# Performance work log

Measured on AMD Instinct MI355X. Metric: run time of the kernel, lower is better.

## Reference

```python
import jax, jax.numpy as jnp
import numpy as np

N_NODES = 50000
N_EDGES = 200000
NODE_DIM = 32   # in_channels (== hidden_dim, required by NNConv nn output size)
EDGE_DIM = 16
HIDDEN = 32
OUT_DIM = 32
EPS = 1e-5
SLOPE = 0.01  # LeakyReLU default negative_slope


def setup_inputs() -> dict:
    key = jax.random.key(0)
    ks = jax.random.split(key, 16)
    inp = {
        "x": jax.random.normal(ks[0], (N_NODES, NODE_DIM), dtype=jnp.float32),
        "edge_index": jax.random.randint(ks[1], (2, N_EDGES), 0, N_NODES, dtype=jnp.int64),
        "edge_attr": jax.random.normal(ks[2], (N_EDGES, EDGE_DIM), dtype=jnp.float32),
        "batch": jnp.zeros((N_NODES,), dtype=jnp.int64),
        # edge MLP params
        "W1": jax.random.normal(ks[3], (EDGE_DIM, HIDDEN), dtype=jnp.float32) / np.sqrt(EDGE_DIM),
        "b1": jnp.zeros((HIDDEN,), dtype=jnp.float32),
        "bn1_gamma": jnp.ones((HIDDEN,), dtype=jnp.float32),
        "bn1_beta": jnp.zeros((HIDDEN,), dtype=jnp.float32),
        "bn1_mean": jax.random.normal(ks[4], (HIDDEN,), dtype=jnp.float32) * 0.1,
        "bn1_var": jax.random.uniform(ks[5], (HIDDEN,), dtype=jnp.float32, minval=0.5, maxval=1.5),
        "W2": jax.random.normal(ks[6], (HIDDEN, HIDDEN * OUT_DIM), dtype=jnp.float32) / np.sqrt(HIDDEN),
        "b2": jnp.zeros((HIDDEN * OUT_DIM,), dtype=jnp.float32),
        "bn2_gamma": jnp.ones((HIDDEN * OUT_DIM,), dtype=jnp.float32),
        "bn2_beta": jnp.zeros((HIDDEN * OUT_DIM,), dtype=jnp.float32),
        "bn2_mean": jax.random.normal(ks[7], (HIDDEN * OUT_DIM,), dtype=jnp.float32) * 0.1,
        "bn2_var": jax.random.uniform(ks[8], (HIDDEN * OUT_DIM,), dtype=jnp.float32, minval=0.5, maxval=1.5),
        # NNConv root weight + bias
        "root": jax.random.normal(ks[9], (NODE_DIM, OUT_DIM), dtype=jnp.float32) / np.sqrt(NODE_DIM),
        "bias": jnp.zeros((OUT_DIM,), dtype=jnp.float32),
    }
    return inp


def _leaky_relu(h):
    return jnp.where(h >= 0, h, SLOPE * h)


def _bn_eval(h, gamma, beta, mean, var):
    return (h - mean) * (gamma / jnp.sqrt(var + EPS)) + beta


def reference(x, edge_index, edge_attr, batch, W1, b1, bn1_gamma, bn1_beta, bn1_mean, bn1_var,
              W2, b2, bn2_gamma, bn2_beta, bn2_mean, bn2_var, root, bias):
    n_nodes = x.shape[0]
    # edge MLP (Dropout is identity in eval mode)
    h = edge_attr @ W1 + b1                                   # [E, H]
    h = _leaky_relu(_bn_eval(h, bn1_gamma, bn1_beta, bn1_mean, bn1_var))
    w = h @ W2 + b2                                           # [E, H*O]
    w = _leaky_relu(_bn_eval(w, bn2_gamma, bn2_beta, bn2_mean, bn2_var))
    w = w.reshape(-1, NODE_DIM, OUT_DIM)                      # [E, in, out]
    # gather source node features, per-edge bmm, scatter-add to destinations
    src, dst = edge_index[0], edge_index[1]
    x_j = x[src]                                              # [E, in]
    msg = jnp.einsum('ei,eio->eo', x_j, w)                    # [E, out]
    aggr = jax.ops.segment_sum(msg, dst, num_segments=n_nodes)
    return aggr + x @ root + bias
```

## Files before the change

kernel.cpp:

```cpp
#include <hip/hip_runtime.h>
#include <math.h>

#define ED 16
#define HD 32
#define OD 32
#define KD 1024
#define EPB 512
#define TPW 4
#define HPAD 34

typedef float  f32x4  __attribute__((ext_vector_type(4)));
typedef float  v4f    __attribute__((ext_vector_type(4)));
typedef short  bf16x8 __attribute__((ext_vector_type(8)));

constexpr size_t WS_BYTES = 71808;

constexpr int LOFF_HX   = 0;
constexpr int LOFF_WHI  = EPB * HPAD * 2;
constexpr int LOFF_W1T  = LOFF_WHI + 32768;
constexpr int LOFF_B1   = LOFF_W1T + 2048;
constexpr int LOFF_BF   = LOFF_B1 + 128;
constexpr int LOFF_SRC  = LOFF_BF + 2048;
constexpr int LOFF_DST  = LOFF_SRC + 2048;
constexpr int LDS_TOTAL = LOFF_DST + 2048;

__device__ inline unsigned short bf16_rne(float v) {
    unsigned int u = __float_as_uint(v);
    return (unsigned short)((u + 0x7FFFu + ((u >> 16) & 1u)) >> 16);
}

__global__ __launch_bounds__(256)
void prep_root_kernel(const float* __restrict__ x, const float* __restrict__ root,
                      const float* __restrict__ bias, float* __restrict__ out, int nN,
                      int nRootBlk,
                      const float* __restrict__ W1, const float* __restrict__ b1,
                      const float* __restrict__ g1, const float* __restrict__ be1,
                      const float* __restrict__ m1, const float* __restrict__ v1,
                      const float* __restrict__ W2, const float* __restrict__ b2,
                      const float* __restrict__ g2, const float* __restrict__ be2,
                      const float* __restrict__ m2, const float* __restrict__ v2,
                      unsigned char* __restrict__ wsb)
{
    const int t = threadIdx.x;
    if ((int)blockIdx.x >= nRootBlk) {
        float* w1t = (float*)(wsb);
        float* b1f = (float*)(wsb + 2048);
        float* bf  = (float*)(wsb + 2176);
        unsigned short* ahi = (unsigned short*)(wsb + 6272);

        int bt = ((int)blockIdx.x - nRootBlk) * blockDim.x + t;
        int stride = 128 * blockDim.x;

        for (int q = bt; q < HD * ED; q += stride) {
            int c = q >> 4, j = q & 15;
            float s = g1[c] / sqrtf(v1[c] + 1e-5f);
            w1t[q] = W1[j * HD + c] * s;
        }
        for (int c = bt; c < HD; c += stride) {
            float s = g1[c] / sqrtf(v1[c] + 1e-5f);
            b1f[c] = b1[c] * s + be1[c] - m1[c] * s;
        }
        for (int k = bt; k < KD; k += stride) {
            float s = g2[k] / sqrtf(v2[k] + 1e-5f);
            bf[k] = b2[k] * s + be2[k] - m2[k] * s;
        }
        for (int p = bt; p < KD * HD; p += stride) {
            int j = p >> 10, k = p & 1023;
            float s = g2[k] / sqrtf(v2[k] + 1e-5f);
            float v = W2[p] * s;
            int g = k >> 4, m = k & 15;
            int quad = j >> 3, idx = j & 7;
            int q = g * 512 + (quad * 16 + m) * 8 + idx;
            ahi[q] = bf16_rne(v);
        }
        return;
    }

    __shared__ __align__(16) float rootS[HD * OD];
    __shared__ __align__(16) float biasS[OD];
    __shared__ float xsh[8][HD + 1];

    ((v4f*)rootS)[t] = ((const v4f*)root)[t];
    if (t < 8) ((v4f*)biasS)[t] = ((const v4f*)bias)[t];

    const int nodeBase = blockIdx.x * 8;
    if (t < 64) {
        int nl = t >> 3, q = t & 7;
        int node = nodeBase + nl;
        if (node >= nN) node = nN - 1;
        v4f v = ((const v4f*)(x + (size_t)node * HD))[q];
        xsh[nl][4 * q + 0] = v.x;
        xsh[nl][4 * q + 1] = v.y;
        xsh[nl][4 * q + 2] = v.z;
        xsh[nl][4 * q + 3] = v.w;
    }
    __syncthreads();

    const int nl = t >> 5, o = t & 31;
    const int node = nodeBase + nl;
    if (node >= nN) return;
    float acc = biasS[o];
#pragma unroll
    for (int i = 0; i < HD; ++i)
        acc = fmaf(xsh[nl][i], rootS[i * OD + o], acc);
    out[(size_t)node * OD + o] = acc;
}

__global__ __launch_bounds__(512, 4)
void edge_kernel(const float* __restrict__ x, const int* __restrict__ eidx,
                 const float* __restrict__ ea_g, const unsigned char* __restrict__ wsb,
                 float* __restrict__ out, int nE)
{
    __shared__ __align__(16) unsigned char smem[LDS_TOTAL];
    unsigned short* hHi = (unsigned short*)(smem + LOFF_HX);
    unsigned short* xS  = (unsigned short*)(smem + LOFF_HX);
    unsigned short* wLhi = (unsigned short*)(smem + LOFF_WHI);
    float* w1t = (float*)(smem + LOFF_W1T);
    float* b1s = (float*)(smem + LOFF_B1);
    float* bfL = (float*)(smem + LOFF_BF);
    int*  srcS = (int*)(smem + LOFF_SRC);
    int*  dstS = (int*)(smem + LOFF_DST);

    const int t = threadIdx.x;
    const int s = blockIdx.y;
    const float* wsW1 = (const float*)(wsb);
    const float* wsB1 = (const float*)(wsb + 2048);
    const float* wsBf = (const float*)(wsb + 2176);
    const unsigned short* wsAhi = (const unsigned short*)(wsb + 6272);

    int e = blockIdx.x * EPB + t;
    int ec = (e < nE) ? e : (nE - 1);
    int my_src = __builtin_nontemporal_load(eidx + ec);
    int my_dst = __builtin_nontemporal_load(eidx + nE + ec);

    const v4f* xrow_p = (const v4f*)(x + (size_t)my_src * HD);
    v4f xrow[8];
#pragma unroll
    for (int q = 0; q < 8; ++q) xrow[q] = xrow_p[q];

    const v4f* eap = (const v4f*)(ea_g + (size_t)ec * ED);
    v4f a0 = __builtin_nontemporal_load(eap + 0);
    v4f a1 = __builtin_nontemporal_load(eap + 1);
    v4f a2 = __builtin_nontemporal_load(eap + 2);
    v4f a3 = __builtin_nontemporal_load(eap + 3);

    srcS[t] = my_src;
    dstS[t] = my_dst;

    if (t < 128)       ((v4f*)w1t)[t] = ((const v4f*)wsW1)[t];
    else if (t < 136)  ((v4f*)b1s)[t - 128] = ((const v4f*)wsB1)[t - 128];
    else if (t < 264) {
        int d = t - 136;
        ((v4f*)bfL)[d] = ((const v4f*)wsBf)[(d >> 2) * 8 + s * 4 + (d & 3)];
    }

    {
        const v4f* srcHi = (const v4f*)wsAhi;
        v4f* dstHi = (v4f*)wLhi;
#pragma unroll
        for (int p = 0; p < 4; ++p) {
            int c = t + p * 512;
            int sc = (2 * (c >> 6) + s) * 64 + (c & 63);
            dstHi[c] = srcHi[sc];
        }
    }

    __syncthreads();

    float hreg[HD];
#pragma unroll
    for (int c = 0; c < HD; ++c) {
        const v4f* r4 = (const v4f*)(w1t + c * ED);
        v4f w0 = r4[0], w1 = r4[1], w2 = r4[2], w3 = r4[3];
        float acc = b1s[c];
        acc = fmaf(a0.x, w0.x, acc); acc = fmaf(a0.y, w0.y, acc);
        acc = fmaf(a0.z, w0.z, acc); acc = fmaf(a0.w, w0.w, acc);
        acc = fmaf(a1.x, w1.x, acc); acc = fmaf(a1.y, w1.y, acc);
        acc = fmaf(a1.z, w1.z, acc); acc = fmaf(a1.w, w1.w, acc);
        acc = fmaf(a2.x, w2.x, acc); acc = fmaf(a2.y, w2.y, acc);
        acc = fmaf(a2.z, w2.z, acc); acc = fmaf(a2.w, w2.w, acc);
        acc = fmaf(a3.x, w3.x, acc); acc = fmaf(a3.y, w3.y, acc);
        acc = fmaf(a3.z, w3.z, acc); acc = fmaf(a3.w, w3.w, acc);
        hreg[c] = fmaxf(acc, 0.01f * acc);
    }

#pragma unroll
    for (int ch = 0; ch < 4; ++ch) {
        bf16x8 phi;
#pragma unroll
        for (int u = 0; u < 8; ++u)
            phi[u] = (short)bf16_rne(hreg[ch * 8 + u]);
        *(bf16x8*)(hHi + t * HPAD + ch * 8) = phi;
    }
    __syncthreads();

    const int wave = t >> 6;
    const int lane = t & 63;
    const int n = lane & 15;
    const int quad = lane >> 4;
    const int ebase = wave * 64;

    bf16x8 bHi[TPW];
#pragma unroll
    for (int tt = 0; tt < TPW; ++tt) {
        int edge = ebase + tt * 16 + n;
        bHi[tt] = *(const bf16x8*)(hHi + edge * HPAD + quad * 8);
    }

    int xdst[TPW];
    bool evalid[TPW];
    int xoff[TPW];
#pragma unroll
    for (int tt = 0; tt < TPW; ++tt) {
        int le = ebase + tt * 16 + n;
        evalid[tt] = (blockIdx.x * EPB + le) < nE;
        xdst[tt] = dstS[le];
        xoff[tt] = le * HPAD;
    }

    __syncthreads();

#pragma unroll
    for (int ch = 0; ch < 4; ++ch) {
        bf16x8 px;
#pragma unroll
        for (int u = 0; u < 8; ++u) {
            int q = ch * 2 + (u >> 2);
            px[u] = (short)bf16_rne(xrow[q][u & 3]);
        }
        *(bf16x8*)(xS + t * HPAD + ch * 8) = px;
    }
    __syncthreads();

    f32x4 msg[TPW];
#pragma unroll
    for (int tt = 0; tt < TPW; ++tt)
        msg[tt] = (f32x4){0.f, 0.f, 0.f, 0.f};

#pragma unroll 4
    for (int i = 0; i < HD; ++i) {
        const bf16x8 cH = *(const bf16x8*)(wLhi + i * 512 + lane * 8);
        const f32x4 b0 = *(const f32x4*)(bfL + i * 16 + quad * 4);
        float xv[TPW];
#pragma unroll
        for (int tt = 0; tt < TPW; ++tt) {
            unsigned int u = xS[xoff[tt] + i];
            xv[tt] = __uint_as_float(u << 16);
        }

#pragma unroll
        for (int tt = 0; tt < TPW; ++tt) {
            f32x4 c = b0;
            c = __builtin_amdgcn_mfma_f32_16x16x32_bf16(cH, bHi[tt], c, 0, 0, 0);
            f32x4 w = __builtin_elementwise_max(c, 0.01f * c);
            f32x4 xs = {xv[tt], xv[tt], xv[tt], xv[tt]};
            msg[tt] = __builtin_elementwise_fma(xs, w, msg[tt]);
        }
    }

#pragma unroll
    for (int tt = 0; tt < TPW; ++tt) {
        if (!evalid[tt]) continue;
        float* op = out + (size_t)xdst[tt] * OD + s * 16 + quad * 4;
#pragma unroll
        for (int r = 0; r < 4; ++r)
            atomicAdd(op + r, msg[tt][r]);
    }
}

__global__ __launch_bounds__(64)
void edge_kernel_raw(const float* __restrict__ x, const int* __restrict__ eidx,
                     const float* __restrict__ ea_g,
                     const float* __restrict__ W1, const float* __restrict__ b1,
                     const float* __restrict__ g1, const float* __restrict__ be1,
                     const float* __restrict__ m1, const float* __restrict__ v1,
                     const float* __restrict__ W2, const float* __restrict__ b2,
                     const float* __restrict__ g2, const float* __restrict__ be2,
                     const float* __restrict__ m2, const float* __restrict__ v2,
                     float* __restrict__ out, int nE)
{
    int e = blockIdx.x * 64 + threadIdx.x;
    if (e >= nE) return;
    const int obase = blockIdx.y * 16;

    int src = eidx[e];
    int dst = eidx[nE + e];

    float ea[ED];
#pragma unroll
    for (int j = 0; j < ED; ++j) ea[j] = ea_g[(size_t)e * ED + j];

    float h[HD];
#pragma unroll
    for (int c = 0; c < HD; ++c) {
        float acc = b1[c];
#pragma unroll
        for (int j = 0; j < ED; ++j) acc = fmaf(ea[j], W1[j * HD + c], acc);
        float s = g1[c] / sqrtf(v1[c] + 1e-5f);
        acc = (acc - m1[c]) * s + be1[c];
        h[c] = fmaxf(acc, 0.01f * acc);
    }

    float msg[16];
#pragma unroll
    for (int o = 0; o < 16; ++o) msg[o] = 0.f;

    const float* xj = x + (size_t)src * HD;
    for (int i = 0; i < HD; ++i) {
        float xv = xj[i];
#pragma unroll
        for (int oo = 0; oo < 16; ++oo) {
            int k = i * OD + obase + oo;
            float acc = b2[k];
#pragma unroll
            for (int j = 0; j < HD; ++j) acc = fmaf(h[j], W2[j * KD + k], acc);
            float s = g2[k] / sqrtf(v2[k] + 1e-5f);
            acc = (acc - m2[k]) * s + be2[k];
            float w = fmaxf(acc, 0.01f * acc);
            msg[oo] = fmaf(xv, w, msg[oo]);
        }
    }

    float* op = out + (size_t)dst * OD + obase;
#pragma unroll
    for (int oo = 0; oo < 16; ++oo) atomicAdd(op + oo, msg[oo]);
}

extern "C" void kernel_launch(void* const* d_in, const int* in_sizes, int n_in,
                              void* d_out, int out_size, void* d_ws, size_t ws_size,
                              hipStream_t stream)
{
    const float* x    = (const float*)d_in[0];
    const int*   eidx = (const int*)  d_in[1];
    const float* ea   = (const float*)d_in[2];
    const float* W1   = (const float*)d_in[4];
    const float* b1   = (const float*)d_in[5];
    const float* g1   = (const float*)d_in[6];
    const float* be1  = (const float*)d_in[7];
    const float* m1   = (const float*)d_in[8];
    const float* v1   = (const float*)d_in[9];
    const float* W2   = (const float*)d_in[10];
    const float* b2   = (const float*)d_in[11];
    const float* g2   = (const float*)d_in[12];
    const float* be2  = (const float*)d_in[13];
    const float* m2   = (const float*)d_in[14];
    const float* v2   = (const float*)d_in[15];
    const float* root = (const float*)d_in[16];
    const float* bias = (const float*)d_in[17];
    float* out = (float*)d_out;

    int nN = in_sizes[0] / HD;
    int nE = in_sizes[2] / ED;

    if (ws_size >= WS_BYTES) {
        unsigned char* wsb = (unsigned char*)d_ws;
        int nRootBlk = (nN + 7) / 8;
        prep_root_kernel<<<dim3(nRootBlk + 128), 256, 0, stream>>>(
            x, root, bias, out, nN, nRootBlk,
            W1, b1, g1, be1, m1, v1, W2, b2, g2, be2, m2, v2, wsb);
        int nblk = (nE + EPB - 1) / EPB;
        edge_kernel<<<dim3(nblk, 2), 512, 0, stream>>>(x, eidx, ea, wsb, out, nE);
    } else {
        prep_root_kernel<<<dim3((nN + 7) / 8), 256, 0, stream>>>(
            x, root, bias, out, nN, (nN + 7) / 8 + 1,
            W1, b1, g1, be1, m1, v1, W2, b2, g2, be2, m2, v2, (unsigned char*)d_ws);
        edge_kernel_raw<<<dim3((nE + 63) / 64, 2), 64, 0, stream>>>(
            x, eidx, ea, W1, b1, g1, be1, m1, v1,
            W2, b2, g2, be2, m2, v2, out, nE);
    }
}
```

Measured before the change: 215.3 us.

## Replace atomic scatter with message buffer plus per-destination bucketed gather

The edge kernel now writes each edge's message to a workspace buffer with nontemporal stores instead of issuing float atomics into the output. A bucket kernel assigns edges to per-destination slots, capped at CAP and falling back to atomics on overflow, and a gather kernel sums the bucketed messages per node. This aims to remove contention and traffic from many scattered float atomics. The cost is three extra launches, about 25 MB of message buffer written and read back, and one int atomic per edge. The path is only taken when the workspace is large enough.

```diff
diff --git a/kernel.cpp b/kernel.cpp
--- a/kernel.cpp
+++ b/kernel.cpp
@@ -8,12 +8,14 @@
 #define EPB 512
 #define TPW 4
 #define HPAD 34
+#define CAP 32
 
 typedef float  f32x4  __attribute__((ext_vector_type(4)));
 typedef float  v4f    __attribute__((ext_vector_type(4)));
 typedef short  bf16x8 __attribute__((ext_vector_type(8)));
 
-constexpr size_t WS_BYTES = 71808;
+constexpr size_t WS_WEIGHTS = 71808;
+constexpr size_t OFF_MSG = 72064;
 
 constexpr int LOFF_HX   = 0;
 constexpr int LOFF_WHI  = EPB * HPAD * 2;
@@ -106,10 +108,11 @@
     out[(size_t)node * OD + o] = acc;
 }
 
+template <bool MSG>
 __global__ __launch_bounds__(512, 4)
 void edge_kernel(const float* __restrict__ x, const int* __restrict__ eidx,
                  const float* __restrict__ ea_g, const unsigned char* __restrict__ wsb,
-                 float* __restrict__ out, int nE)
+                 float* __restrict__ outm, int nE)
 {
     __shared__ __align__(16) unsigned char smem[LDS_TOTAL];
     unsigned short* hHi = (unsigned short*)(smem + LOFF_HX);
@@ -210,10 +213,12 @@
     int xdst[TPW];
     bool evalid[TPW];
     int xoff[TPW];
+    int geid[TPW];
 #pragma unroll
     for (int tt = 0; tt < TPW; ++tt) {
         int le = ebase + tt * 16 + n;
-        evalid[tt] = (blockIdx.x * EPB + le) < nE;
+        geid[tt] = blockIdx.x * EPB + le;
+        evalid[tt] = geid[tt] < nE;
         xdst[tt] = dstS[le];
         xoff[tt] = le * HPAD;
     }
@@ -258,14 +263,67 @@
         }
     }
 
-#pragma unroll
-    for (int tt = 0; tt < TPW; ++tt) {
-        if (!evalid[tt]) continue;
-        float* op = out + (size_t)xdst[tt] * OD + s * 16 + quad * 4;
-#pragma unroll
-        for (int r = 0; r < 4; ++r)
-            atomicAdd(op + r, msg[tt][r]);
-    }
+    if (MSG) {
+#pragma unroll
+        for (int tt = 0; tt < TPW; ++tt) {
+            if (!evalid[tt]) continue;
+            float* mp = outm + (size_t)geid[tt] * OD + s * 16 + quad * 4;
+            __builtin_nontemporal_store(msg[tt], (f32x4*)mp);
+        }
+    } else {
+#pragma unroll
+        for (int tt = 0; tt < TPW; ++tt) {
+            if (!evalid[tt]) continue;
+            float* op = outm + (size_t)xdst[tt] * OD + s * 16 + quad * 4;
+#pragma unroll
+            for (int r = 0; r < 4; ++r)
+                atomicAdd(op + r, msg[tt][r]);
+        }
+    }
+}
+
+__global__ void zero_cnt_kernel(int* __restrict__ cnt, int nN)
+{
+    int t = blockIdx.x * blockDim.x + threadIdx.x;
+    if (t < nN) cnt[t] = 0;
+}
+
+__global__ void bucket_kernel(const int* __restrict__ eidx,
+                              const float* __restrict__ msg,
+                              float* __restrict__ out,
+                              int* __restrict__ cnt, int* __restrict__ bucket, int nE)
+{
+    int e = blockIdx.x * blockDim.x + threadIdx.x;
+    if (e >= nE) return;
+    int dst = eidx[nE + e];
+    int pos = atomicAdd(cnt + dst, 1);
+    if (pos < CAP) {
+        bucket[(size_t)dst * CAP + pos] = e;
+    } else {
+        const float* mp = msg + (size_t)e * OD;
+        float* op = out + (size_t)dst * OD;
+#pragma unroll
+        for (int ch = 0; ch < OD; ++ch) atomicAdd(op + ch, mp[ch]);
+    }
+}
+
+__global__ __launch_bounds__(256)
+void gather_kernel(const float* __restrict__ msg, const int* __restrict__ bucket,
+                   const int* __restrict__ cnt, float* __restrict__ out, int nN)
+{
+    int t = threadIdx.x;
+    int v = blockIdx.x * 8 + (t >> 5);
+    int ch = t & 31;
+    if (v >= nN) return;
+    int c = cnt[v];
+    if (c > CAP) c = CAP;
+    const int* bk = bucket + (size_t)v * CAP;
+    float acc = 0.f;
+    for (int p = 0; p < c; ++p) {
+        int e = bk[p];
+        acc += msg[(size_t)e * OD + ch];
+    }
+    out[(size_t)v * OD + ch] += acc;
 }
 
 __global__ __launch_bounds__(64)
@@ -352,14 +410,35 @@
     int nN = in_sizes[0] / HD;
     int nE = in_sizes[2] / ED;
 
-    if (ws_size >= WS_BYTES) {
+    size_t msgB = (size_t)nE * OD * 4;
+    size_t bktB = (size_t)nN * CAP * 4;
+    size_t OFF_BKT = OFF_MSG + msgB;
+    size_t OFF_CNT = OFF_BKT + bktB;
+    size_t needTwoPhase = OFF_CNT + (size_t)nN * 4;
+
+    if (ws_size >= needTwoPhase) {
+        unsigned char* wsb = (unsigned char*)d_ws;
+        float* msg  = (float*)(wsb + OFF_MSG);
+        int* bucket = (int*)(wsb + OFF_BKT);
+        int* cnt    = (int*)(wsb + OFF_CNT);
+
+        int nRootBlk = (nN + 7) / 8;
+        prep_root_kernel<<<dim3(nRootBlk + 128), 256, 0, stream>>>(
+            x, root, bias, out, nN, nRootBlk,
+            W1, b1, g1, be1, m1, v1, W2, b2, g2, be2, m2, v2, wsb);
+        zero_cnt_kernel<<<(nN + 1023) / 1024, 1024, 0, stream>>>(cnt, nN);
+        int nblk = (nE + EPB - 1) / EPB;
+        edge_kernel<true><<<dim3(nblk, 2), 512, 0, stream>>>(x, eidx, ea, wsb, msg, nE);
+        bucket_kernel<<<(nE + 255) / 256, 256, 0, stream>>>(eidx, msg, out, cnt, bucket, nE);
+        gather_kernel<<<(nN + 7) / 8, 256, 0, stream>>>(msg, bucket, cnt, out, nN);
+    } else if (ws_size >= WS_WEIGHTS) {
         unsigned char* wsb = (unsigned char*)d_ws;
         int nRootBlk = (nN + 7) / 8;
         prep_root_kernel<<<dim3(nRootBlk + 128), 256, 0, stream>>>(
             x, root, bias, out, nN, nRootBlk,
             W1, b1, g1, be1, m1, v1, W2, b2, g2, be2, m2, v2, wsb);
         int nblk = (nE + EPB - 1) / EPB;
-        edge_kernel<<<dim3(nblk, 2), 512, 0, stream>>>(x, eidx, ea, wsb, out, nE);
+        edge_kernel<false><<<dim3(nblk, 2), 512, 0, stream>>>(x, eidx, ea, wsb, out, nE);
     } else {
         prep_root_kernel<<<dim3((nN + 7) / 8), 256, 0, stream>>>(
             x, root, bias, out, nN, (nN + 7) / 8 + 1,
```

Result: faster. 203.9 us (-5.3%).

## Fuse into cooperative kernel with bucketed gather instead of float atomics

Applied to the files above, without the earlier changes.

Replaces the prep/root kernel plus atomic-scatter edge kernel with one persistent cooperative kernel. Each block stages the BN-folded weights itself, edge messages are written to a bf16 buffer, and edges are bucketed per destination node. After a grid sync, each node sums its bucket together with the root term. This removes the separate prep launch and the float atomicAdd traffic on the output. In exchange it adds two grid syncs, a bucket atomic per edge, an extra message buffer round trip, bf16 rounding of messages, and a slow linear-scan fallback for nodes with more than CAP incoming edges.

```diff
diff --git a/kernel.cpp b/kernel.cpp
--- a/kernel.cpp
+++ b/kernel.cpp
@@ -1,5 +1,8 @@
 #include <hip/hip_runtime.h>
+#include <hip/hip_cooperative_groups.h>
 #include <math.h>
+
+namespace cg = cooperative_groups;
 
 #define ED 16
 #define HD 32
@@ -8,127 +11,88 @@
 #define EPB 512
 #define TPW 4
 #define HPAD 34
+#define CAP 32
 
 typedef float  f32x4  __attribute__((ext_vector_type(4)));
 typedef float  v4f    __attribute__((ext_vector_type(4)));
 typedef short  bf16x8 __attribute__((ext_vector_type(8)));
-
-constexpr size_t WS_BYTES = 71808;
-
-constexpr int LOFF_HX   = 0;
-constexpr int LOFF_WHI  = EPB * HPAD * 2;
-constexpr int LOFF_W1T  = LOFF_WHI + 32768;
-constexpr int LOFF_B1   = LOFF_W1T + 2048;
-constexpr int LOFF_BF   = LOFF_B1 + 128;
-constexpr int LOFF_SRC  = LOFF_BF + 2048;
-constexpr int LOFF_DST  = LOFF_SRC + 2048;
-constexpr int LDS_TOTAL = LOFF_DST + 2048;
+typedef short  bf16x4 __attribute__((ext_vector_type(4)));
+
+constexpr int LOFF_HX  = 0;
+constexpr int LOFF_WHI = EPB * HPAD * 2;
+constexpr int LOFF_W1T = LOFF_WHI + 32768;
+constexpr int LOFF_B1  = LOFF_W1T + 2048;
+constexpr int LOFF_BF  = LOFF_B1 + 128;
+constexpr int LOFF_DST = LOFF_BF + 2048;
+constexpr int LDS_TOTAL= LOFF_DST + 2048;
 
 __device__ inline unsigned short bf16_rne(float v) {
     unsigned int u = __float_as_uint(v);
     return (unsigned short)((u + 0x7FFFu + ((u >> 16) & 1u)) >> 16);
 }
 
-__global__ __launch_bounds__(256)
-void prep_root_kernel(const float* __restrict__ x, const float* __restrict__ root,
-                      const float* __restrict__ bias, float* __restrict__ out, int nN,
-                      int nRootBlk,
-                      const float* __restrict__ W1, const float* __restrict__ b1,
-                      const float* __restrict__ g1, const float* __restrict__ be1,
-                      const float* __restrict__ m1, const float* __restrict__ v1,
-                      const float* __restrict__ W2, const float* __restrict__ b2,
-                      const float* __restrict__ g2, const float* __restrict__ be2,
-                      const float* __restrict__ m2, const float* __restrict__ v2,
-                      unsigned char* __restrict__ wsb)
-{
-    const int t = threadIdx.x;
-    if ((int)blockIdx.x >= nRootBlk) {
-        float* w1t = (float*)(wsb);
-        float* b1f = (float*)(wsb + 2048);
-        float* bf  = (float*)(wsb + 2176);
-        unsigned short* ahi = (unsigned short*)(wsb + 6272);
-
-        int bt = ((int)blockIdx.x - nRootBlk) * blockDim.x + t;
-        int stride = 128 * blockDim.x;
-
-        for (int q = bt; q < HD * ED; q += stride) {
-            int c = q >> 4, j = q & 15;
-            float s = g1[c] / sqrtf(v1[c] + 1e-5f);
-            w1t[q] = W1[j * HD + c] * s;
-        }
-        for (int c = bt; c < HD; c += stride) {
-            float s = g1[c] / sqrtf(v1[c] + 1e-5f);
-            b1f[c] = b1[c] * s + be1[c] - m1[c] * s;
-        }
-        for (int k = bt; k < KD; k += stride) {
-            float s = g2[k] / sqrtf(v2[k] + 1e-5f);
-            bf[k] = b2[k] * s + be2[k] - m2[k] * s;
-        }
-        for (int p = bt; p < KD * HD; p += stride) {
-            int j = p >> 10, k = p & 1023;
-            float s = g2[k] / sqrtf(v2[k] + 1e-5f);
-            float v = W2[p] * s;
-            int g = k >> 4, m = k & 15;
-            int quad = j >> 3, idx = j & 7;
-            int q = g * 512 + (quad * 16 + m) * 8 + idx;
-            ahi[q] = bf16_rne(v);
-        }
-        return;
-    }
-
-    __shared__ __align__(16) float rootS[HD * OD];
-    __shared__ __align__(16) float biasS[OD];
-    __shared__ float xsh[8][HD + 1];
-
-    ((v4f*)rootS)[t] = ((const v4f*)root)[t];
-    if (t < 8) ((v4f*)biasS)[t] = ((const v4f*)bias)[t];
-
-    const int nodeBase = blockIdx.x * 8;
-    if (t < 64) {
-        int nl = t >> 3, q = t & 7;
-        int node = nodeBase + nl;
-        if (node >= nN) node = nN - 1;
-        v4f v = ((const v4f*)(x + (size_t)node * HD))[q];
-        xsh[nl][4 * q + 0] = v.x;
-        xsh[nl][4 * q + 1] = v.y;
-        xsh[nl][4 * q + 2] = v.z;
-        xsh[nl][4 * q + 3] = v.w;
-    }
-    __syncthreads();
-
-    const int nl = t >> 5, o = t & 31;
-    const int node = nodeBase + nl;
-    if (node >= nN) return;
-    float acc = biasS[o];
-#pragma unroll
-    for (int i = 0; i < HD; ++i)
-        acc = fmaf(xsh[nl][i], rootS[i * OD + o], acc);
-    out[(size_t)node * OD + o] = acc;
-}
-
-__global__ __launch_bounds__(512, 4)
-void edge_kernel(const float* __restrict__ x, const int* __restrict__ eidx,
-                 const float* __restrict__ ea_g, const unsigned char* __restrict__ wsb,
-                 float* __restrict__ out, int nE)
-{
-    __shared__ __align__(16) unsigned char smem[LDS_TOTAL];
-    unsigned short* hHi = (unsigned short*)(smem + LOFF_HX);
-    unsigned short* xS  = (unsigned short*)(smem + LOFF_HX);
-    unsigned short* wLhi = (unsigned short*)(smem + LOFF_WHI);
+__device__ __forceinline__ void stage_weights(
+    int t, int s, unsigned char* smem,
+    const float* __restrict__ W1, const float* __restrict__ b1,
+    const float* __restrict__ g1, const float* __restrict__ be1,
+    const float* __restrict__ m1, const float* __restrict__ v1,
+    const float* __restrict__ W2, const float* __restrict__ b2,
+    const float* __restrict__ g2, const float* __restrict__ be2,
+    const float* __restrict__ m2, const float* __restrict__ v2)
+{
     float* w1t = (float*)(smem + LOFF_W1T);
     float* b1s = (float*)(smem + LOFF_B1);
     float* bfL = (float*)(smem + LOFF_BF);
-    int*  srcS = (int*)(smem + LOFF_SRC);
-    int*  dstS = (int*)(smem + LOFF_DST);
-
-    const int t = threadIdx.x;
-    const int s = blockIdx.y;
-    const float* wsW1 = (const float*)(wsb);
-    const float* wsB1 = (const float*)(wsb + 2048);
-    const float* wsBf = (const float*)(wsb + 2176);
-    const unsigned short* wsAhi = (const unsigned short*)(wsb + 6272);
-
-    int e = blockIdx.x * EPB + t;
+    unsigned short* wLhi = (unsigned short*)(smem + LOFF_WHI);
+
+    {
+        int c = t >> 4, j = t & 15;
+        float sc = g1[c] / sqrtf(v1[c] + 1e-5f);
+        w1t[t] = W1[j * HD + c] * sc;
+    }
+    if (t < HD) {
+        float sc = g1[t] / sqrtf(v1[t] + 1e-5f);
+        b1s[t] = b1[t] * sc + be1[t] - m1[t] * sc;
+    }
+    {
+        int i = t >> 4, m = t & 15;
+        int k = (2 * i + s) * 16 + m;
+        float sc = g2[k] / sqrtf(v2[k] + 1e-5f);
+        bfL[t] = b2[k] * sc + be2[k] - m2[k] * sc;
+    }
+#pragma unroll
+    for (int p = 0; p < 4; ++p) {
+        int c = t + p * 512;
+        int i = c >> 6, ln = c & 63;
+        int m = ln & 15, quad = ln >> 4;
+        int k = (2 * i + s) * 16 + m;
+        float sc = g2[k] / sqrtf(v2[k] + 1e-5f);
+        bf16x8 w;
+#pragma unroll
+        for (int idx = 0; idx < 8; ++idx) {
+            int j = quad * 8 + idx;
+            w[idx] = (short)bf16_rne(W2[j * KD + k] * sc);
+        }
+        *(bf16x8*)(wLhi + (size_t)c * 8) = w;
+    }
+}
+
+__device__ __forceinline__ void edge_tile(
+    int t, int s, int tileBase, unsigned char* smem,
+    const float* __restrict__ x, const int* __restrict__ eidx,
+    const float* __restrict__ ea_g,
+    unsigned short* __restrict__ msgb, int* __restrict__ cnt,
+    int* __restrict__ bucket, int nE)
+{
+    unsigned short* hHi = (unsigned short*)(smem + LOFF_HX);
+    unsigned short* xS  = (unsigned short*)(smem + LOFF_HX);
+    const unsigned short* wLhi = (const unsigned short*)(smem + LOFF_WHI);
+    const float* w1t = (const float*)(smem + LOFF_W1T);
+    const float* b1s = (const float*)(smem + LOFF_B1);
+    const float* bfL = (const float*)(smem + LOFF_BF);
+    int* dstS = (int*)(smem + LOFF_DST);
+
+    int e = tileBase + t;
     int ec = (e < nE) ? e : (nE - 1);
     int my_src = __builtin_nontemporal_load(eidx + ec);
     int my_dst = __builtin_nontemporal_load(eidx + nE + ec);
@@ -144,28 +108,7 @@
     v4f a2 = __builtin_nontemporal_load(eap + 2);
     v4f a3 = __builtin_nontemporal_load(eap + 3);
 
-    srcS[t] = my_src;
     dstS[t] = my_dst;
-
-    if (t < 128)       ((v4f*)w1t)[t] = ((const v4f*)wsW1)[t];
-    else if (t < 136)  ((v4f*)b1s)[t - 128] = ((const v4f*)wsB1)[t - 128];
-    else if (t < 264) {
-        int d = t - 136;
-        ((v4f*)bfL)[d] = ((const v4f*)wsBf)[(d >> 2) * 8 + s * 4 + (d & 3)];
-    }
-
-    {
-        const v4f* srcHi = (const v4f*)wsAhi;
-        v4f* dstHi = (v4f*)wLhi;
-#pragma unroll
-        for (int p = 0; p < 4; ++p) {
-            int c = t + p * 512;
-            int sc = (2 * (c >> 6) + s) * 64 + (c & 63);
-            dstHi[c] = srcHi[sc];
-        }
-    }
-
-    __syncthreads();
 
     float hreg[HD];
 #pragma unroll
@@ -184,6 +127,8 @@
         hreg[c] = fmaxf(acc, 0.01f * acc);
     }
 
+    __syncthreads();
+
 #pragma unroll
     for (int ch = 0; ch < 4; ++ch) {
         bf16x8 phi;
@@ -210,10 +155,12 @@
     int xdst[TPW];
     bool evalid[TPW];
     int xoff[TPW];
+    int geid[TPW];
 #pragma unroll
     for (int tt = 0; tt < TPW; ++tt) {
         int le = ebase + tt * 16 + n;
-        evalid[tt] = (blockIdx.x * EPB + le) < nE;
+        geid[tt] = tileBase + le;
+        evalid[tt] = geid[tt] < nE;
         xdst[tt] = dstS[le];
         xoff[tt] = le * HPAD;
     }
@@ -247,7 +194,6 @@
             unsigned int u = xS[xoff[tt] + i];
             xv[tt] = __uint_as_float(u << 16);
         }
-
 #pragma unroll
         for (int tt = 0; tt < TPW; ++tt) {
             f32x4 c = b0;
@@ -261,50 +207,203 @@
 #pragma unroll
     for (int tt = 0; tt < TPW; ++tt) {
         if (!evalid[tt]) continue;
-        float* op = out + (size_t)xdst[tt] * OD + s * 16 + quad * 4;
-#pragma unroll
-        for (int r = 0; r < 4; ++r)
-            atomicAdd(op + r, msg[tt][r]);
-    }
+        bf16x4 pm;
+#pragma unroll
+        for (int r = 0; r < 4; ++r) pm[r] = (short)bf16_rne(msg[tt][r]);
+        __builtin_nontemporal_store(pm,
+            (bf16x4*)(msgb + (size_t)geid[tt] * OD + s * 16 + quad * 4));
+    }
+    if (s == 0 && quad == 0) {
+#pragma unroll
+        for (int tt = 0; tt < TPW; ++tt) {
+            if (!evalid[tt]) continue;
+            int pos = atomicAdd(cnt + xdst[tt], 1);
+            if (pos < CAP) bucket[(size_t)xdst[tt] * CAP + pos] = geid[tt];
+        }
+    }
+}
+
+__device__ __forceinline__ void gather_phase(
+    int t, unsigned char* smem,
+    const float* __restrict__ x, const float* __restrict__ root,
+    const float* __restrict__ bias,
+    const unsigned short* __restrict__ msgb,
+    const int* __restrict__ bucket, const int* __restrict__ cnt,
+    const int* __restrict__ eidx,
+    float* __restrict__ out, int nN, int nE, int bx, int gdx)
+{
+    float* rootS = (float*)smem;
+    float* biasS = (float*)(smem + 4096);
+    float* xsh   = (float*)(smem + 4224);
+
+    if (t < 256)      ((v4f*)rootS)[t] = ((const v4f*)root)[t];
+    else if (t < 264) ((v4f*)biasS)[t - 256] = ((const v4f*)bias)[t - 256];
+
+    int nGroups = (nN + 15) / 16;
+    for (int grp = bx; grp < nGroups; grp += gdx) {
+        __syncthreads();
+        if (t < 128) {
+            int nl = t >> 3, q = t & 7;
+            int node = grp * 16 + nl;
+            if (node >= nN) node = nN - 1;
+            v4f v = ((const v4f*)(x + (size_t)node * HD))[q];
+            xsh[nl * 33 + 4 * q + 0] = v.x;
+            xsh[nl * 33 + 4 * q + 1] = v.y;
+            xsh[nl * 33 + 4 * q + 2] = v.z;
+            xsh[nl * 33 + 4 * q + 3] = v.w;
+        }
+        __syncthreads();
+
+        int nl = t >> 5, ch = t & 31;
+        int v = grp * 16 + nl;
+        if (v < nN) {
+            float acc = biasS[ch];
+#pragma unroll
+            for (int i = 0; i < HD; ++i)
+                acc = fmaf(xsh[nl * 33 + i], rootS[i * OD + ch], acc);
+            int c = cnt[v];
+            if (c <= CAP) {
+                const int* bk = bucket + (size_t)v * CAP;
+                for (int p = 0; p < c; ++p) {
+                    int e = bk[p];
+                    unsigned int u = msgb[(size_t)e * OD + ch];
+                    acc += __uint_as_float(u << 16);
+                }
+            } else {
+                const int* dstp = eidx + nE;
+                for (int e = 0; e < nE; ++e)
+                    if (dstp[e] == v) {
+                        unsigned int u = msgb[(size_t)e * OD + ch];
+                        acc += __uint_as_float(u << 16);
+                    }
+            }
+            __builtin_nontemporal_store(acc, out + (size_t)v * OD + ch);
+        }
+    }
+}
+
+__global__ __launch_bounds__(512, 4)
+void fused_kernel(const float* __restrict__ x, const int* __restrict__ eidx,
+                  const float* __restrict__ ea,
+                  const float* __restrict__ W1, const float* __restrict__ b1,
+                  const float* __restrict__ g1, const float* __restrict__ be1,
+                  const float* __restrict__ m1, const float* __restrict__ v1,
+                  const float* __restrict__ W2, const float* __restrict__ b2,
+                  const float* __restrict__ g2, const float* __restrict__ be2,
+                  const float* __restrict__ m2, const float* __restrict__ v2,
+                  const float* __restrict__ root, const float* __restrict__ bias,
+                  unsigned short* msgb, int* bucket, int* cnt,
+                  float* out, int nN, int nE)
+{
+    __shared__ __align__(16) unsigned char smem[LDS_TOTAL];
+    const int t = threadIdx.x;
+    const int s = (int)blockIdx.x & 1;
+
+    for (int i = (int)blockIdx.x * 512 + t; i < nN; i += (int)gridDim.x * 512)
+        atomicExch(cnt + i, 0);
+
+    stage_weights(t, s, smem, W1, b1, g1, be1, m1, v1,
+                  W2, b2, g2, be2, m2, v2);
+
+    cg::this_grid().sync();
+
+    const int nTiles = (nE + EPB - 1) / EPB;
+    for (int tile = (int)blockIdx.x >> 1; tile < nTiles; tile += (int)gridDim.x >> 1)
+        edge_tile(t, s, tile * EPB, smem, x, eidx, ea, msgb, cnt, bucket, nE);
+
+    __threadfence();
+    cg::this_grid().sync();
+
+    gather_phase(t, smem, x, root, bias, msgb, bucket, cnt, eidx,
+                 out, nN, nE, (int)blockIdx.x, (int)gridDim.x);
+}
+
+__global__ void zero_cnt_k(int* __restrict__ cnt, int nN)
+{
+    int i = blockIdx.x * blockDim.x + threadIdx.x;
+    if (i < nN) cnt[i] = 0;
+}
+
+__global__ __launch_bounds__(512, 4)
+void edge_k(const float* __restrict__ x, const int* __restrict__ eidx,
+            const float* __restrict__ ea,
+            const float* __restrict__ W1, const float* __restrict__ b1,
+            const float* __restrict__ g1, const float* __restrict__ be1,
+            const float* __restrict__ m1, const float* __restrict__ v1,
+            const float* __restrict__ W2, const float* __restrict__ b2,
+            const float* __restrict__ g2, const float* __restrict__ be2,
+            const float* __restrict__ m2, const float* __restrict__ v2,
+            unsigned short* msgb, int* cnt, int* bucket, int nE)
+{
+    __shared__ __align__(16) unsigned char smem[LDS_TOTAL];
+    const int t = threadIdx.x;
+    const int s = blockIdx.y;
+    stage_weights(t, s, smem, W1, b1, g1, be1, m1, v1,
+                  W2, b2, g2, be2, m2, v2);
+    __syncthreads();
+    edge_tile(t, s, (int)blockIdx.x * EPB, smem, x, eidx, ea, msgb, cnt, bucket, nE);
+}
+
+__global__ __launch_bounds__(512)
+void gather_k(const float* __restrict__ x, const float* __restrict__ root,
+              const float* __restrict__ bias,
+              const unsigned short* __restrict__ msgb,
+              const int* __restrict__ bucket, const int* __restrict__ cnt,
+              const int* __restrict__ eidx,
+              float* __restrict__ out, int nN, int nE)
+{
+    __shared__ __align__(16) unsigned char smem[4224 + 16 * 33 * 4];
+    gather_phase(threadIdx.x, smem, x, root, bias, msgb, bucket, cnt, eidx,
+                 out, nN, nE, (int)blockIdx.x, (int)gridDim.x);
+}
+
+__global__ void root_init_k(const float* __restrict__ x, const float* __restrict__ root,
+                            const float* __restrict__ bias, float* __restrict__ out, int nN)
+{
+    int t = blockIdx.x * blockDim.x + threadIdx.x;
+    if (t >= nN * OD) return;
+    int o = t & (OD - 1);
+    int n = t >> 5;
+    const float* xr = x + (size_t)n * HD;
+    float acc = bias[o];
+#pragma unroll
+    for (int i = 0; i < HD; ++i)
+        acc = fmaf(xr[i], root[i * OD + o], acc);
+    out[t] = acc;
 }
 
 __global__ __launch_bounds__(64)
-void edge_kernel_raw(const float* __restrict__ x, const int* __restrict__ eidx,
-                     const float* __restrict__ ea_g,
-                     const float* __restrict__ W1, const float* __restrict__ b1,
-                     const float* __restrict__ g1, const float* __restrict__ be1,
-                     const float* __restrict__ m1, const float* __restrict__ v1,
-                     const float* __restrict__ W2, const float* __restrict__ b2,
-                     const float* __restrict__ g2, const float* __restrict__ be2,
-                     const float* __restrict__ m2, const float* __restrict__ v2,
-                     float* __restrict__ out, int nE)
+void edge_raw_k(const float* __restrict__ x, const int* __restrict__ eidx,
+                const float* __restrict__ ea_g,
+                const float* __restrict__ W1, const float* __restrict__ b1,
+                const float* __restrict__ g1, const float* __restrict__ be1,
+                const float* __restrict__ m1, const float* __restrict__ v1,
+                const float* __restrict__ W2, const float* __restrict__ b2,
+                const float* __restrict__ g2, const float* __restrict__ be2,
+                const float* __restrict__ m2, const float* __restrict__ v2,
+                float* __restrict__ out, int nE)
 {
     int e = blockIdx.x * 64 + threadIdx.x;
     if (e >= nE) return;
     const int obase = blockIdx.y * 16;
-
     int src = eidx[e];
     int dst = eidx[nE + e];
-
-    float ea[ED];
-#pragma unroll
-    for (int j = 0; j < ED; ++j) ea[j] = ea_g[(size_t)e * ED + j];
-
+    float eav[ED];
+#pragma unroll
+    for (int j = 0; j < ED; ++j) eav[j] = ea_g[(size_t)e * ED + j];
     float h[HD];
 #pragma unroll
     for (int c = 0; c < HD; ++c) {
         float acc = b1[c];
 #pragma unroll
-        for (int j = 0; j < ED; ++j) acc = fmaf(ea[j], W1[j * HD + c], acc);
-        float s = g1[c] / sqrtf(v1[c] + 1e-5f);
-        acc = (acc - m1[c]) * s + be1[c];
+        for (int j = 0; j < ED; ++j) acc = fmaf(eav[j], W1[j * HD + c], acc);
+        float sc = g1[c] / sqrtf(v1[c] + 1e-5f);
+        acc = (acc - m1[c]) * sc + be1[c];
         h[c] = fmaxf(acc, 0.01f * acc);
     }
-
     float msg[16];
 #pragma unroll
     for (int o = 0; o < 16; ++o) msg[o] = 0.f;
-
     const float* xj = x + (size_t)src * HD;
     for (int i = 0; i < HD; ++i) {
         float xv = xj[i];
@@ -314,13 +413,12 @@
             float acc = b2[k];
 #pragma unroll
             for (int j = 0; j < HD; ++j) acc = fmaf(h[j], W2[j * KD + k], acc);
-            float s = g2[k] / sqrtf(v2[k] + 1e-5f);
-            acc = (acc - m2[k]) * s + be2[k];
+            float sc = g2[k] / sqrtf(v2[k] + 1e-5f);
+            acc = (acc - m2[k]) * sc + be2[k];
             float w = fmaxf(acc, 0.01f * acc);
             msg[oo] = fmaf(xv, w, msg[oo]);
         }
     }
-
     float* op = out + (size_t)dst * OD + obase;
 #pragma unroll
     for (int oo = 0; oo < 16; ++oo) atomicAdd(op + oo, msg[oo]);
@@ -352,19 +450,57 @@
     int nN = in_sizes[0] / HD;
     int nE = in_sizes[2] / ED;
 
-    if (ws_size >= WS_BYTES) {
+    size_t msgB = (size_t)nE * OD * 2;
+    size_t OFF_BKT = (msgB + 15) & ~(size_t)15;
+    size_t OFF_CNT = OFF_BKT + (size_t)nN * CAP * 4;
+    size_t need = OFF_CNT + (size_t)nN * 4;
+
+    if (ws_size >= need) {
         unsigned char* wsb = (unsigned char*)d_ws;
-        int nRootBlk = (nN + 7) / 8;
-        prep_root_kernel<<<dim3(nRootBlk + 128), 256, 0, stream>>>(
-            x, root, bias, out, nN, nRootBlk,
-            W1, b1, g1, be1, m1, v1, W2, b2, g2, be2, m2, v2, wsb);
-        int nblk = (nE + EPB - 1) / EPB;
-        edge_kernel<<<dim3(nblk, 2), 512, 0, stream>>>(x, eidx, ea, wsb, out, nE);
+        unsigned short* msgb = (unsigned short*)wsb;
+        int* bucket = (int*)(wsb + OFF_BKT);
+        int* cnt    = (int*)(wsb + OFF_CNT);
+
+        bool launched = false;
+        int occ = 0;
+        hipError_t e1 = hipOccupancyMaxActiveBlocksPerMultiprocessor(
+            &occ, (const void*)fused_kernel, 512, 0);
+        if (e1 == hipSuccess && occ > 0) {
+            int dev = 0;
+            hipGetDevice(&dev);
+            hipDeviceProp_t prop;
+            if (hipGetDeviceProperties(&prop, dev) == hipSuccess) {
+                int grid = occ * prop.multiProcessorCount;
+                grid &= ~1;
+                if (grid >= 2) {
+                    void* args[] = {
+                        (void*)&x, (void*)&eidx, (void*)&ea,
+                        (void*)&W1, (void*)&b1, (void*)&g1, (void*)&be1,
+                        (void*)&m1, (void*)&v1,
+                        (void*)&W2, (void*)&b2, (void*)&g2, (void*)&be2,
+                        (void*)&m2, (void*)&v2,
+                        (void*)&root, (void*)&bias,
+                        (void*)&msgb, (void*)&bucket, (void*)&cnt,
+                        (void*)&out, (void*)&nN, (void*)&nE };
+                    hipError_t e3 = hipLaunchCooperativeKernel(
+                        (const void*)fused_kernel, dim3(grid), dim3(512),
+                        args, 0, stream);
+                    launched = (e3 == hipSuccess);
+                }
+            }
+        }
+        if (!launched) {
+            zero_cnt_k<<<(nN + 511) / 512, 512, 0, stream>>>(cnt, nN);
+            int nTiles = (nE + EPB - 1) / EPB;
+            edge_k<<<dim3(nTiles, 2), 512, 0, stream>>>(
+                x, eidx, ea, W1, b1, g1, be1, m1, v1,
+                W2, b2, g2, be2, m2, v2, msgb, cnt, bucket, nE);
+            gather_k<<<(nN + 15) / 16, 512, 0, stream>>>(
+                x, root, bias, msgb, bucket, cnt, eidx, out, nN, nE);
+        }
     } else {
-        prep_root_kernel<<<dim3((nN + 7) / 8), 256, 0, stream>>>(
-            x, root, bias, out, nN, (nN + 7) / 8 + 1,
-            W1, b1, g1, be1, m1, v1, W2, b2, g2, be2, m2, v2, (unsigned char*)d_ws);
-        edge_kernel_raw<<<dim3((nE + 63) / 64, 2), 64, 0, stream>>>(
+        root_init_k<<<(nN * OD + 255) / 256, 256, 0, stream>>>(x, root, bias, out, nN);
+        edge_raw_k<<<dim3((nE + 63) / 64, 2), 64, 0, stream>>>(
             x, eidx, ea, W1, b1, g1, be1, m1, v1,
             W2, b2, g2, be2, m2, v2, out, nE);
     }
```

Result: slower. 398.9 us (+85.3%).
